# Optimization experiments

Measured on AMD Instinct MI355X. Metric: run time of the kernel, lower is better.

Reference implementation:

```python
import jax, jax.numpy as jnp
import numpy as np


def setup_inputs() -> dict:
    key = jax.random.key(0)
    kx, km = jax.random.split(key)
    B, T, D = 32, 4096, 512
    x = jax.random.normal(kx, (B, T, D), dtype=jnp.float32)
    # mask semantics follow the torch module: True = excluded, kept rows are ~mask
    mask = jax.random.randint(km, (B, T), 0, 2) == 1
    # ensure at least one kept (False) position per row so mean is well-defined
    mask = mask.at[:, 0].set(False)
    return {"x": x, "mask": mask}


def reference(x, mask):
    # masked mean over time: keep positions where mask is False (torch uses v[~m])
    keep = (~mask).astype(x.dtype)                      # [B, T]
    denom = jnp.sum(keep, axis=1, keepdims=True)        # [B, 1]
    pooled = jnp.einsum('btd,bt->bd', x, keep) / denom  # [B, D]
    return pooled
```

## Files before the change

kernel.cpp:

```cpp
#include <hip/hip_runtime.h>


#define BB 32
#define TT 4096
#define DD 512
#define SPLITS 32
#define ROWS_PER_BLOCK (TT / SPLITS)

__global__ __launch_bounds__(256) void masked_pool_partial(
    const float* __restrict__ x, const int* __restrict__ mask,
    float* __restrict__ out)
{
    __shared__ float s_keep[ROWS_PER_BLOCK];
    const int b   = blockIdx.x;
    const int s   = blockIdx.y;
    const int tid = threadIdx.x;
    const int t0  = s * ROWS_PER_BLOCK;

    if (tid < ROWS_PER_BLOCK) {
        s_keep[tid] = (mask[b * TT + t0 + tid] == 0) ? 1.0f : 0.0f;
    }
    __syncthreads();

    const int tx = tid & 127;
    const int ty = tid >> 7;

    const float4* xrow = (const float4*)(x + (size_t)b * TT * DD)
                         + (size_t)t0 * (DD / 4);

    float4 acc = make_float4(0.f, 0.f, 0.f, 0.f);
    #pragma unroll 8
    for (int r = ty; r < ROWS_PER_BLOCK; r += 2) {
        float  k = s_keep[r];
        float4 v = xrow[(size_t)r * (DD / 4) + tx];
        acc.x += k * v.x;
        acc.y += k * v.y;
        acc.z += k * v.z;
        acc.w += k * v.w;
    }

    float* o = out + (size_t)b * DD + tx * 4;
    atomicAdd(o + 0, acc.x);
    atomicAdd(o + 1, acc.y);
    atomicAdd(o + 2, acc.z);
    atomicAdd(o + 3, acc.w);
}

__global__ __launch_bounds__(256) void masked_pool_scale(
    const int* __restrict__ mask, float* __restrict__ out)
{
    const int b   = blockIdx.x;
    const int tid = threadIdx.x;

    int cnt = 0;
    #pragma unroll
    for (int t = tid; t < TT; t += 256) cnt += (mask[b * TT + t] == 0) ? 1 : 0;

    #pragma unroll
    for (int off = 32; off > 0; off >>= 1) cnt += __shfl_down(cnt, off, 64);

    __shared__ int s_cnt[4];
    if ((tid & 63) == 0) s_cnt[tid >> 6] = cnt;
    __syncthreads();

    const int denom = s_cnt[0] + s_cnt[1] + s_cnt[2] + s_cnt[3];
    const float inv = 1.0f / (float)denom;

    for (int d = tid; d < DD; d += 256) out[(size_t)b * DD + d] *= inv;
}

extern "C" void kernel_launch(void* const* d_in, const int* in_sizes, int n_in,
                              void* d_out, int out_size, void* d_ws, size_t ws_size,
                              hipStream_t stream) {
    const float* x    = (const float*)d_in[0];
    const int*   mask = (const int*)d_in[1];
    float*       out  = (float*)d_out;

    hipMemsetAsync(out, 0, (size_t)out_size * sizeof(float), stream);

    dim3 grid(BB, SPLITS);
    masked_pool_partial<<<grid, 256, 0, stream>>>(x, mask, out);
    masked_pool_scale<<<BB, 256, 0, stream>>>(mask, out);
}
```

Measured before the change: 367.6 us.

## Replace atomic accumulation with workspace partials and deterministic reduce kernel

The partial kernel now writes per-split float4 partial sums into a workspace instead of issuing float atomics on the output. A second kernel sums the partials across splits and applies the mask-count scale, so the memset is no longer needed. Splits double to 64 and blocks shrink to 128 threads, with each thread walking all rows of its split. This removes atomic contention and one launch, at the cost of a workspace round-trip and a serial 64-way reduce per column.

```diff
diff --git a/kernel.cpp b/kernel.cpp
--- a/kernel.cpp
+++ b/kernel.cpp
@@ -4,50 +4,43 @@
 #define BB 32
 #define TT 4096
 #define DD 512
-#define SPLITS 32
-#define ROWS_PER_BLOCK (TT / SPLITS)
+#define SPLITS 64
+#define ROWS (TT / SPLITS)
+#define D4 (DD / 4)
 
-__global__ __launch_bounds__(256) void masked_pool_partial(
+__global__ __launch_bounds__(128) void masked_pool_partial(
     const float* __restrict__ x, const int* __restrict__ mask,
-    float* __restrict__ out)
+    float4* __restrict__ ws)
 {
-    __shared__ float s_keep[ROWS_PER_BLOCK];
+    __shared__ float s_keep[ROWS];
     const int b   = blockIdx.x;
     const int s   = blockIdx.y;
     const int tid = threadIdx.x;
-    const int t0  = s * ROWS_PER_BLOCK;
+    const int t0  = s * ROWS;
 
-    if (tid < ROWS_PER_BLOCK) {
+    if (tid < ROWS)
         s_keep[tid] = (mask[b * TT + t0 + tid] == 0) ? 1.0f : 0.0f;
-    }
     __syncthreads();
 
-    const int tx = tid & 127;
-    const int ty = tid >> 7;
-
-    const float4* xrow = (const float4*)(x + (size_t)b * TT * DD)
-                         + (size_t)t0 * (DD / 4);
+    const float4* xp = (const float4*)x + ((size_t)b * TT + t0) * D4 + tid;
 
     float4 acc = make_float4(0.f, 0.f, 0.f, 0.f);
     #pragma unroll 8
-    for (int r = ty; r < ROWS_PER_BLOCK; r += 2) {
-        float  k = s_keep[r];
-        float4 v = xrow[(size_t)r * (DD / 4) + tx];
+    for (int r = 0; r < ROWS; ++r) {
+        const float  k = s_keep[r];
+        const float4 v = xp[(size_t)r * D4];
         acc.x += k * v.x;
         acc.y += k * v.y;
         acc.z += k * v.z;
         acc.w += k * v.w;
     }
 
-    float* o = out + (size_t)b * DD + tx * 4;
-    atomicAdd(o + 0, acc.x);
-    atomicAdd(o + 1, acc.y);
-    atomicAdd(o + 2, acc.z);
-    atomicAdd(o + 3, acc.w);
+    ws[((size_t)b * SPLITS + s) * D4 + tid] = acc;
 }
 
-__global__ __launch_bounds__(256) void masked_pool_scale(
-    const int* __restrict__ mask, float* __restrict__ out)
+__global__ __launch_bounds__(256) void masked_pool_reduce(
+    const float4* __restrict__ ws, const int* __restrict__ mask,
+    float4* __restrict__ out)
 {
     const int b   = blockIdx.x;
     const int tid = threadIdx.x;
@@ -55,18 +48,25 @@
     int cnt = 0;
     #pragma unroll
     for (int t = tid; t < TT; t += 256) cnt += (mask[b * TT + t] == 0) ? 1 : 0;
-
     #pragma unroll
     for (int off = 32; off > 0; off >>= 1) cnt += __shfl_down(cnt, off, 64);
 
     __shared__ int s_cnt[4];
     if ((tid & 63) == 0) s_cnt[tid >> 6] = cnt;
     __syncthreads();
+    const float inv = 1.0f / (float)(s_cnt[0] + s_cnt[1] + s_cnt[2] + s_cnt[3]);
 
-    const int denom = s_cnt[0] + s_cnt[1] + s_cnt[2] + s_cnt[3];
-    const float inv = 1.0f / (float)denom;
-
-    for (int d = tid; d < DD; d += 256) out[(size_t)b * DD + d] *= inv;
+    if (tid < D4) {
+        const float4* p = ws + (size_t)b * SPLITS * D4 + tid;
+        float4 acc = make_float4(0.f, 0.f, 0.f, 0.f);
+        #pragma unroll 8
+        for (int s = 0; s < SPLITS; ++s) {
+            const float4 v = p[(size_t)s * D4];
+            acc.x += v.x; acc.y += v.y; acc.z += v.z; acc.w += v.w;
+        }
+        acc.x *= inv; acc.y *= inv; acc.z *= inv; acc.w *= inv;
+        out[(size_t)b * D4 + tid] = acc;
+    }
 }
 
 extern "C" void kernel_launch(void* const* d_in, const int* in_sizes, int n_in,
@@ -74,11 +74,10 @@
                               hipStream_t stream) {
     const float* x    = (const float*)d_in[0];
     const int*   mask = (const int*)d_in[1];
-    float*       out  = (float*)d_out;
-
-    hipMemsetAsync(out, 0, (size_t)out_size * sizeof(float), stream);
+    float4*      ws   = (float4*)d_ws;
+    float4*      out  = (float4*)d_out;
 
     dim3 grid(BB, SPLITS);
-    masked_pool_partial<<<grid, 256, 0, stream>>>(x, mask, out);
-    masked_pool_scale<<<BB, 256, 0, stream>>>(mask, out);
+    masked_pool_partial<<<grid, 128, 0, stream>>>(x, mask, ws);
+    masked_pool_reduce<<<BB, 256, 0, stream>>>(ws, mask, out);
 }
```

New measurement: 372.0 us. Within noise of the previous version (+1.2%).
